# Kernel optimization log

Hardware: AMD Instinct MI355X
Metric: run time of the kernel (lower is better)

## Reference

```python
import jax, jax.numpy as jnp
import numpy as np

N, C_IN, P, S_D = 8, 512, 64, 512
N_GROUPS = C_IN // P      # 8
C_OUT = C_IN              # c_out defaults to c_in
EPS = 1e-5                # F.instance_norm default
SLOPE = 0.01              # LeakyReLU default


def setup_inputs() -> dict:
    key = jax.random.key(0)
    ks = jax.random.split(key, 8)
    def xavier(k, shape):
        fan_out, fan_in = shape
        std = (2.0 / (fan_in + fan_out)) ** 0.5
        return jax.random.normal(k, shape, dtype=jnp.float32) * std
    return {
        "style_encoding": jax.random.normal(ks[0], (N, S_D, 32, 32), dtype=jnp.float32),
        "predicted": jax.random.normal(ks[1], (N, C_IN, 128, 128), dtype=jnp.float32),
        "W1": xavier(ks[2], (C_IN, S_D)),
        "b1": jnp.full((C_IN,), 0.01, dtype=jnp.float32),
        "W2": xavier(ks[3], (C_OUT * P, C_IN)),
        "b2": jnp.full((C_OUT * P,), 0.01, dtype=jnp.float32),
        "Wb1": xavier(ks[4], (C_IN, S_D)),
        "bb1": jnp.full((C_IN,), 0.01, dtype=jnp.float32),
        "Wb2": xavier(ks[5], (C_OUT, C_IN)),
        "bb2": jnp.full((C_OUT,), 0.01, dtype=jnp.float32),
    }


def _forward(style_encoding, predicted, W1, b1, W2, b2, Wb1, bb1, Wb2, bb2):
    n, c, h, w = predicted.shape
    # AdaptiveAvgPool2d(1): pooled style vector [N, s_d]
    s = jnp.mean(style_encoding, axis=(2, 3))
    # kernel branch: two 1x1 convs on a 1x1 map == two matmuls
    hk = jax.nn.leaky_relu(s @ W1.T + b1, SLOPE)
    kn = hk @ W2.T + b2                      # [N, c_out*p]
    kernel = kn.reshape(n, N_GROUPS, P, P)   # row n*c_out+oc -> (n, oc//p, oc%p, :)
    # bias branch
    hb = jax.nn.leaky_relu(s @ Wb1.T + bb1, SLOPE)
    bias = (hb @ Wb2.T + bb2).reshape(n, N_GROUPS, P)  # [N, n_groups, p]
    # instance norm (no affine, biased variance)
    mu = jnp.mean(predicted, axis=(2, 3), keepdims=True)
    var = jnp.var(predicted, axis=(2, 3), keepdims=True)
    xn = (predicted - mu) * jax.lax.rsqrt(var + EPS)
    # grouped 1x1 conv: per (sample, group) GEMM [p,p] x [p, H*W]
    xg = xn.reshape(n, N_GROUPS, P, h, w)
    out = jnp.einsum("ngop,ngphw->ngohw", kernel, xg) + bias[:, :, :, None, None]
    return out.reshape(n, C_OUT, h, w)


def reference(style_encoding, predicted, W1, b1, W2, b2, Wb1, bb1, Wb2, bb2):
    return _forward(style_encoding, predicted, W1, b1, W2, b2, Wb1, bb1, Wb2, bb2)
```

## Files before the change

### kernel.cpp

```cpp
#include <hip/hip_runtime.h>


typedef __attribute__((ext_vector_type(8))) short bf16x8;
typedef __attribute__((ext_vector_type(4))) float f32x4;

__device__ __forceinline__ float lrelu(float v) { return v > 0.f ? v : 0.01f * v; }

__device__ __forceinline__ unsigned short f2bf(float f) {
    unsigned int u = __float_as_uint(f);
    unsigned int r = (u + 0x7FFFu + ((u >> 16) & 1u)) >> 16;
    return (unsigned short)r;
}

__global__ void k_poolstats(const float* __restrict__ style, const float* __restrict__ x,
                            float* __restrict__ s, float* __restrict__ mu,
                            float* __restrict__ rs) {
    if (blockIdx.x < 1024) {
        int wv = threadIdx.x >> 6, lane = threadIdx.x & 63;
        int b = blockIdx.x * 4 + wv;
        const float4* p4 = (const float4*)(style + (size_t)b * 1024);
        float v = 0.f;
        #pragma unroll
        for (int i = 0; i < 4; ++i) {
            float4 t = p4[lane + 64 * i];
            v += t.x + t.y + t.z + t.w;
        }
        #pragma unroll
        for (int off = 32; off > 0; off >>= 1) v += __shfl_xor(v, off, 64);
        if (lane == 0) s[b] = v * (1.f / 1024.f);
    } else {
        __shared__ float ps[4], pq[4];
        int b = blockIdx.x - 1024;
        int tid = threadIdx.x, wv = tid >> 6, lane = tid & 63;
        const float4* p4 = (const float4*)(x + (size_t)b * 16384);
        float sm = 0.f, q = 0.f;
        #pragma unroll
        for (int i = 0; i < 16; ++i) {
            float4 v = p4[tid + 256 * i];
            sm += v.x + v.y + v.z + v.w;
            q += v.x * v.x + v.y * v.y + v.z * v.z + v.w * v.w;
        }
        #pragma unroll
        for (int off = 32; off > 0; off >>= 1) {
            sm += __shfl_xor(sm, off, 64);
            q  += __shfl_xor(q, off, 64);
        }
        if (lane == 0) { ps[wv] = sm; pq[wv] = q; }
        __syncthreads();
        if (tid == 0) {
            float S = ps[0] + ps[1] + ps[2] + ps[3];
            float Q = pq[0] + pq[1] + pq[2] + pq[3];
            float m = S * (1.f / 16384.f);
            float v = Q * (1.f / 16384.f) - m * m;
            mu[b] = m;
            rs[b] = rsqrtf(v + 1e-5f);
        }
    }
}

__global__ void k_mlp1(const float* __restrict__ s, const float* __restrict__ W1,
                       const float* __restrict__ b1, const float* __restrict__ Wb1,
                       const float* __restrict__ bb1, float* __restrict__ hk,
                       float* __restrict__ hb) {
    __shared__ float sv[4096];
    const float4* s4 = (const float4*)s;
    float4* sv4 = (float4*)sv;
    #pragma unroll
    for (int i = 0; i < 4; ++i) sv4[threadIdx.x + 256 * i] = s4[threadIdx.x + 256 * i];
    __syncthreads();
    int wv = threadIdx.x >> 6, lane = threadIdx.x & 63;
    int row = blockIdx.x * 4 + wv;
    int r2 = row & 511;
    const float* wrow = (row < 512) ? W1 + (size_t)r2 * 512 : Wb1 + (size_t)r2 * 512;
    float bias = (row < 512) ? b1[r2] : bb1[r2];
    float acc[8] = {0.f,0.f,0.f,0.f,0.f,0.f,0.f,0.f};
    #pragma unroll
    for (int c = 0; c < 2; ++c) {
        float4 w4 = *(const float4*)(wrow + lane * 4 + 256 * c);
        #pragma unroll
        for (int n = 0; n < 8; ++n) {
            float4 h4 = *(const float4*)(sv + n * 512 + lane * 4 + 256 * c);
            acc[n] += w4.x * h4.x + w4.y * h4.y + w4.z * h4.z + w4.w * h4.w;
        }
    }
    #pragma unroll
    for (int n = 0; n < 8; ++n) {
        float v = acc[n];
        #pragma unroll
        for (int off = 32; off > 0; off >>= 1) v += __shfl_xor(v, off, 64);
        acc[n] = v;
    }
    if (lane == 0) {
        float* dst = (row < 512) ? hk : hb;
        #pragma unroll
        for (int n = 0; n < 8; ++n) dst[n * 512 + r2] = lrelu(acc[n] + bias);
    }
}

__global__ void k_mlp2(const float* __restrict__ hk, const float* __restrict__ hb,
                       const float* __restrict__ W2, const float* __restrict__ b2,
                       const float* __restrict__ Wb2, const float* __restrict__ bb2,
                       float* __restrict__ kn, float* __restrict__ bvec) {
    __shared__ float h[8192];
    const float4* hk4 = (const float4*)hk;
    const float4* hb4 = (const float4*)hb;
    float4* h4 = (float4*)h;
    #pragma unroll
    for (int i = 0; i < 4; ++i) {
        h4[threadIdx.x + 256 * i]        = hk4[threadIdx.x + 256 * i];
        h4[1024 + threadIdx.x + 256 * i] = hb4[threadIdx.x + 256 * i];
    }
    __syncthreads();
    int wv = threadIdx.x >> 6, lane = threadIdx.x & 63;
    int row = blockIdx.x * 4 + wv;
    const float* wrow;
    const float* hbase;
    float bias;
    int r2 = row - 32768;
    if (row < 32768) { wrow = W2 + (size_t)row * 512; hbase = h; bias = b2[row]; }
    else             { wrow = Wb2 + (size_t)r2 * 512; hbase = h + 4096; bias = bb2[r2]; }
    float acc[8] = {0.f,0.f,0.f,0.f,0.f,0.f,0.f,0.f};
    #pragma unroll
    for (int c = 0; c < 2; ++c) {
        f32x4 w4 = __builtin_nontemporal_load((const f32x4*)(wrow + lane * 4 + 256 * c));
        #pragma unroll
        for (int n = 0; n < 8; ++n) {
            float4 x4 = *(const float4*)(hbase + n * 512 + lane * 4 + 256 * c);
            acc[n] += w4[0] * x4.x + w4[1] * x4.y + w4[2] * x4.z + w4[3] * x4.w;
        }
    }
    #pragma unroll
    for (int n = 0; n < 8; ++n) {
        float v = acc[n];
        #pragma unroll
        for (int off = 32; off > 0; off >>= 1) v += __shfl_xor(v, off, 64);
        acc[n] = v;
    }
    if (lane == 0) {
        if (row < 32768) {
            #pragma unroll
            for (int n = 0; n < 8; ++n) kn[(size_t)n * 32768 + row] = acc[n] + bias;
        } else {
            #pragma unroll
            for (int n = 0; n < 8; ++n) bvec[n * 512 + r2] = acc[n] + bias;
        }
    }
}

__global__ void k_fold(const float* __restrict__ kn, const float* __restrict__ bvec,
                       const float* __restrict__ mu, const float* __restrict__ rs,
                       unsigned short* __restrict__ Kp, float* __restrict__ bp) {
    int wv = threadIdx.x >> 6, lane = threadIdx.x & 63;
    int t = blockIdx.x * 4 + wv;
    int n = t >> 9, rem = t & 511, g = rem >> 6;
    int ci = n * 512 + g * 64 + lane;
    float kv = kn[(size_t)n * 32768 + (size_t)rem * 64 + lane] * rs[ci];
    Kp[(size_t)t * 64 + lane] = f2bf(kv);
    float pm = kv * mu[ci];
    #pragma unroll
    for (int off = 32; off > 0; off >>= 1) pm += __shfl_xor(pm, off, 64);
    if (lane == 0) bp[t] = bvec[n * 512 + rem] - pm;
}

__global__ __launch_bounds__(256) void k_conv(const float* __restrict__ x,
                                              const unsigned short* __restrict__ Kp,
                                              const float* __restrict__ bp,
                                              float* __restrict__ out) {
    int bid = 4095 - (int)blockIdx.x;
    int ng = bid >> 6, slab = bid & 63;
    int wv = threadIdx.x >> 6, lane = threadIdx.x & 63;
    int l15 = lane & 15, lg = lane >> 4;

    const unsigned short* kpb = Kp + (size_t)ng * 4096;
    bf16x8 kfr[4][2];
    #pragma unroll
    for (int ob = 0; ob < 4; ++ob)
        #pragma unroll
        for (int kk = 0; kk < 2; ++kk)
            kfr[ob][kk] = *(const bf16x8*)(kpb + (ob * 16 + l15) * 64 + kk * 32 + lg * 8);

    float bias[4];
    #pragma unroll
    for (int ob = 0; ob < 4; ++ob)
        bias[ob] = bp[ng * 64 + ob * 16 + l15];

    const size_t xbase = (size_t)ng * 64 * 16384;
    int px0 = slab * 256 + wv * 64;

    #pragma unroll
    for (int c = 0; c < 4; ++c) {
        int pxb = px0 + c * 16;
        bf16x8 afr[2];
        #pragma unroll
        for (int kk = 0; kk < 2; ++kk)
            #pragma unroll
            for (int j = 0; j < 8; ++j) {
                int p = kk * 32 + lg * 8 + j;
                afr[kk][j] = (short)f2bf(x[xbase + (size_t)p * 16384 + pxb + l15]);
            }
        #pragma unroll
        for (int ob = 0; ob < 4; ++ob) {
            f32x4 acc = { bias[ob], bias[ob], bias[ob], bias[ob] };
            acc = __builtin_amdgcn_mfma_f32_16x16x32_bf16(afr[0], kfr[ob][0], acc, 0, 0, 0);
            acc = __builtin_amdgcn_mfma_f32_16x16x32_bf16(afr[1], kfr[ob][1], acc, 0, 0, 0);
            f32x4* dst = (f32x4*)(out + (size_t)(ng * 64 + ob * 16 + l15) * 16384 + pxb + lg * 4);
            __builtin_nontemporal_store(acc, dst);
        }
    }
}

extern "C" void kernel_launch(void* const* d_in, const int* in_sizes, int n_in,
                              void* d_out, int out_size, void* d_ws, size_t ws_size,
                              hipStream_t stream) {
    const float* style = (const float*)d_in[0];
    const float* pred  = (const float*)d_in[1];
    const float* W1    = (const float*)d_in[2];
    const float* b1    = (const float*)d_in[3];
    const float* W2    = (const float*)d_in[4];
    const float* b2    = (const float*)d_in[5];
    const float* Wb1   = (const float*)d_in[6];
    const float* bb1   = (const float*)d_in[7];
    const float* Wb2   = (const float*)d_in[8];
    const float* bb2   = (const float*)d_in[9];
    float* out = (float*)d_out;

    float* ws   = (float*)d_ws;
    float* s    = ws;
    float* hk   = s + 4096;
    float* hb   = hk + 4096;
    float* kn   = hb + 4096;
    float* bvec = kn + 262144;
    float* mu   = bvec + 4096;
    float* rs   = mu + 4096;
    float* bp   = rs + 4096;
    unsigned short* Kp = (unsigned short*)(bp + 4096);

    k_poolstats<<<5120, 256, 0, stream>>>(style, pred, s, mu, rs);
    k_mlp1     <<<256,  256, 0, stream>>>(s, W1, b1, Wb1, bb1, hk, hb);
    k_mlp2     <<<8320, 256, 0, stream>>>(hk, hb, W2, b2, Wb2, bb2, kn, bvec);
    k_fold     <<<1024, 256, 0, stream>>>(kn, bvec, mu, rs, Kp, bp);
    k_conv     <<<4096, 256, 0, stream>>>(pred, Kp, bp, out);
}
```

Before: 194.8 us.

## Move instance-norm stats into mlp2 kernel and stage conv output through LDS

The predicted-tensor statistics blocks now run in the same launch as the large W2 GEMV instead of alongside the style pooling. This lets both memory-bound phases overlap, and the small pool kernel finishes earlier. The conv kernel now writes MFMA results into a padded per-wave LDS buffer, then reads them back so each row is stored as a contiguous 128-byte chunk, replacing the scattered 16-byte stores. The cost is extra LDS traffic, about 36KB of LDS per block which may lower occupancy, and a larger mlp2 kernel that keeps 32KB of shared memory even in the stats blocks.

```diff
diff --git a/kernel.cpp b/kernel.cpp
--- a/kernel.cpp
+++ b/kernel.cpp
@@ -12,26 +12,114 @@
     return (unsigned short)r;
 }
 
-__global__ void k_poolstats(const float* __restrict__ style, const float* __restrict__ x,
-                            float* __restrict__ s, float* __restrict__ mu,
-                            float* __restrict__ rs) {
-    if (blockIdx.x < 1024) {
-        int wv = threadIdx.x >> 6, lane = threadIdx.x & 63;
-        int b = blockIdx.x * 4 + wv;
-        const float4* p4 = (const float4*)(style + (size_t)b * 1024);
-        float v = 0.f;
+__global__ void k_pool(const float* __restrict__ style, float* __restrict__ s) {
+    int wv = threadIdx.x >> 6, lane = threadIdx.x & 63;
+    int b = blockIdx.x * 4 + wv;
+    const float4* p4 = (const float4*)(style + (size_t)b * 1024);
+    float v = 0.f;
+    #pragma unroll
+    for (int i = 0; i < 4; ++i) {
+        float4 t = p4[lane + 64 * i];
+        v += t.x + t.y + t.z + t.w;
+    }
+    #pragma unroll
+    for (int off = 32; off > 0; off >>= 1) v += __shfl_xor(v, off, 64);
+    if (lane == 0) s[b] = v * (1.f / 1024.f);
+}
+
+__global__ void k_mlp1(const float* __restrict__ s, const float* __restrict__ W1,
+                       const float* __restrict__ b1, const float* __restrict__ Wb1,
+                       const float* __restrict__ bb1, float* __restrict__ hk,
+                       float* __restrict__ hb) {
+    __shared__ float sv[4096];
+    const float4* s4 = (const float4*)s;
+    float4* sv4 = (float4*)sv;
+    #pragma unroll
+    for (int i = 0; i < 4; ++i) sv4[threadIdx.x + 256 * i] = s4[threadIdx.x + 256 * i];
+    __syncthreads();
+    int wv = threadIdx.x >> 6, lane = threadIdx.x & 63;
+    int row = blockIdx.x * 4 + wv;
+    int r2 = row & 511;
+    const float* wrow = (row < 512) ? W1 + (size_t)r2 * 512 : Wb1 + (size_t)r2 * 512;
+    float bias = (row < 512) ? b1[r2] : bb1[r2];
+    float acc[8] = {0.f,0.f,0.f,0.f,0.f,0.f,0.f,0.f};
+    #pragma unroll
+    for (int c = 0; c < 2; ++c) {
+        float4 w4 = *(const float4*)(wrow + lane * 4 + 256 * c);
+        #pragma unroll
+        for (int n = 0; n < 8; ++n) {
+            float4 h4 = *(const float4*)(sv + n * 512 + lane * 4 + 256 * c);
+            acc[n] += w4.x * h4.x + w4.y * h4.y + w4.z * h4.z + w4.w * h4.w;
+        }
+    }
+    #pragma unroll
+    for (int n = 0; n < 8; ++n) {
+        float v = acc[n];
+        #pragma unroll
+        for (int off = 32; off > 0; off >>= 1) v += __shfl_xor(v, off, 64);
+        acc[n] = v;
+    }
+    if (lane == 0) {
+        float* dst = (row < 512) ? hk : hb;
+        #pragma unroll
+        for (int n = 0; n < 8; ++n) dst[n * 512 + r2] = lrelu(acc[n] + bias);
+    }
+}
+
+__global__ void k_mlp2stats(const float* __restrict__ hk, const float* __restrict__ hb,
+                            const float* __restrict__ W2, const float* __restrict__ b2,
+                            const float* __restrict__ Wb2, const float* __restrict__ bb2,
+                            const float* __restrict__ x,
+                            float* __restrict__ kn, float* __restrict__ bvec,
+                            float* __restrict__ mu, float* __restrict__ rs) {
+    __shared__ float h[8192];
+    __shared__ float ps[4], pq[4];
+    int tid = threadIdx.x, wv = tid >> 6, lane = tid & 63;
+    if (blockIdx.x < 8320) {
+        const float4* hk4 = (const float4*)hk;
+        const float4* hb4 = (const float4*)hb;
+        float4* h4 = (float4*)h;
         #pragma unroll
         for (int i = 0; i < 4; ++i) {
-            float4 t = p4[lane + 64 * i];
-            v += t.x + t.y + t.z + t.w;
-        }
-        #pragma unroll
-        for (int off = 32; off > 0; off >>= 1) v += __shfl_xor(v, off, 64);
-        if (lane == 0) s[b] = v * (1.f / 1024.f);
+            h4[tid + 256 * i]        = hk4[tid + 256 * i];
+            h4[1024 + tid + 256 * i] = hb4[tid + 256 * i];
+        }
+        __syncthreads();
+        int row = blockIdx.x * 4 + wv;
+        const float* wrow;
+        const float* hbase;
+        float bias;
+        int r2 = row - 32768;
+        if (row < 32768) { wrow = W2 + (size_t)row * 512; hbase = h; bias = b2[row]; }
+        else             { wrow = Wb2 + (size_t)r2 * 512; hbase = h + 4096; bias = bb2[r2]; }
+        float acc[8] = {0.f,0.f,0.f,0.f,0.f,0.f,0.f,0.f};
+        #pragma unroll
+        for (int c = 0; c < 2; ++c) {
+            f32x4 w4 = __builtin_nontemporal_load((const f32x4*)(wrow + lane * 4 + 256 * c));
+            #pragma unroll
+            for (int n = 0; n < 8; ++n) {
+                float4 x4 = *(const float4*)(hbase + n * 512 + lane * 4 + 256 * c);
+                acc[n] += w4[0] * x4.x + w4[1] * x4.y + w4[2] * x4.z + w4[3] * x4.w;
+            }
+        }
+        #pragma unroll
+        for (int n = 0; n < 8; ++n) {
+            float v = acc[n];
+            #pragma unroll
+            for (int off = 32; off > 0; off >>= 1) v += __shfl_xor(v, off, 64);
+            acc[n] = v;
+        }
+        if (lane == 0) {
+            if (row < 32768) {
+                #pragma unroll
+                for (int n = 0; n < 8; ++n) kn[(size_t)n * 32768 + row] = acc[n] + bias;
+            } else {
+                #pragma unroll
+                for (int n = 0; n < 8; ++n) bvec[n * 512 + r2] = acc[n] + bias;
+            }
+        }
     } else {
-        __shared__ float ps[4], pq[4];
-        int b = blockIdx.x - 1024;
-        int tid = threadIdx.x, wv = tid >> 6, lane = tid & 63;
+        int b = blockIdx.x - 8320;
         const float4* p4 = (const float4*)(x + (size_t)b * 16384);
         float sm = 0.f, q = 0.f;
         #pragma unroll
@@ -58,95 +146,6 @@
     }
 }
 
-__global__ void k_mlp1(const float* __restrict__ s, const float* __restrict__ W1,
-                       const float* __restrict__ b1, const float* __restrict__ Wb1,
-                       const float* __restrict__ bb1, float* __restrict__ hk,
-                       float* __restrict__ hb) {
-    __shared__ float sv[4096];
-    const float4* s4 = (const float4*)s;
-    float4* sv4 = (float4*)sv;
-    #pragma unroll
-    for (int i = 0; i < 4; ++i) sv4[threadIdx.x + 256 * i] = s4[threadIdx.x + 256 * i];
-    __syncthreads();
-    int wv = threadIdx.x >> 6, lane = threadIdx.x & 63;
-    int row = blockIdx.x * 4 + wv;
-    int r2 = row & 511;
-    const float* wrow = (row < 512) ? W1 + (size_t)r2 * 512 : Wb1 + (size_t)r2 * 512;
-    float bias = (row < 512) ? b1[r2] : bb1[r2];
-    float acc[8] = {0.f,0.f,0.f,0.f,0.f,0.f,0.f,0.f};
-    #pragma unroll
-    for (int c = 0; c < 2; ++c) {
-        float4 w4 = *(const float4*)(wrow + lane * 4 + 256 * c);
-        #pragma unroll
-        for (int n = 0; n < 8; ++n) {
-            float4 h4 = *(const float4*)(sv + n * 512 + lane * 4 + 256 * c);
-            acc[n] += w4.x * h4.x + w4.y * h4.y + w4.z * h4.z + w4.w * h4.w;
-        }
-    }
-    #pragma unroll
-    for (int n = 0; n < 8; ++n) {
-        float v = acc[n];
-        #pragma unroll
-        for (int off = 32; off > 0; off >>= 1) v += __shfl_xor(v, off, 64);
-        acc[n] = v;
-    }
-    if (lane == 0) {
-        float* dst = (row < 512) ? hk : hb;
-        #pragma unroll
-        for (int n = 0; n < 8; ++n) dst[n * 512 + r2] = lrelu(acc[n] + bias);
-    }
-}
-
-__global__ void k_mlp2(const float* __restrict__ hk, const float* __restrict__ hb,
-                       const float* __restrict__ W2, const float* __restrict__ b2,
-                       const float* __restrict__ Wb2, const float* __restrict__ bb2,
-                       float* __restrict__ kn, float* __restrict__ bvec) {
-    __shared__ float h[8192];
-    const float4* hk4 = (const float4*)hk;
-    const float4* hb4 = (const float4*)hb;
-    float4* h4 = (float4*)h;
-    #pragma unroll
-    for (int i = 0; i < 4; ++i) {
-        h4[threadIdx.x + 256 * i]        = hk4[threadIdx.x + 256 * i];
-        h4[1024 + threadIdx.x + 256 * i] = hb4[threadIdx.x + 256 * i];
-    }
-    __syncthreads();
-    int wv = threadIdx.x >> 6, lane = threadIdx.x & 63;
-    int row = blockIdx.x * 4 + wv;
-    const float* wrow;
-    const float* hbase;
-    float bias;
-    int r2 = row - 32768;
-    if (row < 32768) { wrow = W2 + (size_t)row * 512; hbase = h; bias = b2[row]; }
-    else             { wrow = Wb2 + (size_t)r2 * 512; hbase = h + 4096; bias = bb2[r2]; }
-    float acc[8] = {0.f,0.f,0.f,0.f,0.f,0.f,0.f,0.f};
-    #pragma unroll
-    for (int c = 0; c < 2; ++c) {
-        f32x4 w4 = __builtin_nontemporal_load((const f32x4*)(wrow + lane * 4 + 256 * c));
-        #pragma unroll
-        for (int n = 0; n < 8; ++n) {
-            float4 x4 = *(const float4*)(hbase + n * 512 + lane * 4 + 256 * c);
-            acc[n] += w4[0] * x4.x + w4[1] * x4.y + w4[2] * x4.z + w4[3] * x4.w;
-        }
-    }
-    #pragma unroll
-    for (int n = 0; n < 8; ++n) {
-        float v = acc[n];
-        #pragma unroll
-        for (int off = 32; off > 0; off >>= 1) v += __shfl_xor(v, off, 64);
-        acc[n] = v;
-    }
-    if (lane == 0) {
-        if (row < 32768) {
-            #pragma unroll
-            for (int n = 0; n < 8; ++n) kn[(size_t)n * 32768 + row] = acc[n] + bias;
-        } else {
-            #pragma unroll
-            for (int n = 0; n < 8; ++n) bvec[n * 512 + r2] = acc[n] + bias;
-        }
-    }
-}
-
 __global__ void k_fold(const float* __restrict__ kn, const float* __restrict__ bvec,
                        const float* __restrict__ mu, const float* __restrict__ rs,
                        unsigned short* __restrict__ Kp, float* __restrict__ bp) {
@@ -166,10 +165,12 @@
                                               const unsigned short* __restrict__ Kp,
                                               const float* __restrict__ bp,
                                               float* __restrict__ out) {
+    __shared__ float obuf[4][64 * 36];
     int bid = 4095 - (int)blockIdx.x;
     int ng = bid >> 6, slab = bid & 63;
     int wv = threadIdx.x >> 6, lane = threadIdx.x & 63;
     int l15 = lane & 15, lg = lane >> 4;
+    int l8 = lane & 7, lo = lane >> 3;
 
     const unsigned short* kpb = Kp + (size_t)ng * 4096;
     bf16x8 kfr[4][2];
@@ -186,25 +187,35 @@
 
     const size_t xbase = (size_t)ng * 64 * 16384;
     int px0 = slab * 256 + wv * 64;
-
-    #pragma unroll
-    for (int c = 0; c < 4; ++c) {
-        int pxb = px0 + c * 16;
-        bf16x8 afr[2];
-        #pragma unroll
-        for (int kk = 0; kk < 2; ++kk)
-            #pragma unroll
-            for (int j = 0; j < 8; ++j) {
-                int p = kk * 32 + lg * 8 + j;
-                afr[kk][j] = (short)f2bf(x[xbase + (size_t)p * 16384 + pxb + l15]);
+    float* obw = obuf[wv];
+
+    #pragma unroll
+    for (int cp = 0; cp < 2; ++cp) {
+        #pragma unroll
+        for (int c = 0; c < 2; ++c) {
+            int pxb = px0 + cp * 32 + c * 16;
+            bf16x8 afr[2];
+            #pragma unroll
+            for (int kk = 0; kk < 2; ++kk)
+                #pragma unroll
+                for (int j = 0; j < 8; ++j) {
+                    int p = kk * 32 + lg * 8 + j;
+                    afr[kk][j] = (short)f2bf(x[xbase + (size_t)p * 16384 + pxb + l15]);
+                }
+            #pragma unroll
+            for (int ob = 0; ob < 4; ++ob) {
+                f32x4 acc = { bias[ob], bias[ob], bias[ob], bias[ob] };
+                acc = __builtin_amdgcn_mfma_f32_16x16x32_bf16(afr[0], kfr[ob][0], acc, 0, 0, 0);
+                acc = __builtin_amdgcn_mfma_f32_16x16x32_bf16(afr[1], kfr[ob][1], acc, 0, 0, 0);
+                *(f32x4*)(obw + (ob * 16 + l15) * 36 + c * 16 + lg * 4) = acc;
             }
-        #pragma unroll
-        for (int ob = 0; ob < 4; ++ob) {
-            f32x4 acc = { bias[ob], bias[ob], bias[ob], bias[ob] };
-            acc = __builtin_amdgcn_mfma_f32_16x16x32_bf16(afr[0], kfr[ob][0], acc, 0, 0, 0);
-            acc = __builtin_amdgcn_mfma_f32_16x16x32_bf16(afr[1], kfr[ob][1], acc, 0, 0, 0);
-            f32x4* dst = (f32x4*)(out + (size_t)(ng * 64 + ob * 16 + l15) * 16384 + pxb + lg * 4);
-            __builtin_nontemporal_store(acc, dst);
+        }
+        #pragma unroll
+        for (int i = 0; i < 8; ++i) {
+            int o = i * 8 + lo;
+            f32x4 v = *(const f32x4*)(obw + o * 36 + l8 * 4);
+            f32x4* dst = (f32x4*)(out + (size_t)(ng * 64 + o) * 16384 + px0 + cp * 32 + l8 * 4);
+            __builtin_nontemporal_store(v, dst);
         }
     }
 }
@@ -235,9 +246,9 @@
     float* bp   = rs + 4096;
     unsigned short* Kp = (unsigned short*)(bp + 4096);
 
-    k_poolstats<<<5120, 256, 0, stream>>>(style, pred, s, mu, rs);
-    k_mlp1     <<<256,  256, 0, stream>>>(s, W1, b1, Wb1, bb1, hk, hb);
-    k_mlp2     <<<8320, 256, 0, stream>>>(hk, hb, W2, b2, Wb2, bb2, kn, bvec);
-    k_fold     <<<1024, 256, 0, stream>>>(kn, bvec, mu, rs, Kp, bp);
-    k_conv     <<<4096, 256, 0, stream>>>(pred, Kp, bp, out);
-}
+    k_pool     <<<1024,  256, 0, stream>>>(style, s);
+    k_mlp1     <<<256,   256, 0, stream>>>(s, W1, b1, Wb1, bb1, hk, hb);
+    k_mlp2stats<<<12416, 256, 0, stream>>>(hk, hb, W2, b2, Wb2, bb2, pred, kn, bvec, mu, rs);
+    k_fold     <<<1024,  256, 0, stream>>>(kn, bvec, mu, rs, Kp, bp);
+    k_conv     <<<4096,  256, 0, stream>>>(pred, Kp, bp, out);
+}
```

New measurement: 167.9 us. -13.8%, faster.
